# Optimization experiments

Hardware: AMD Instinct MI355X
Metric: run time of the kernel (lower is better)

## Reference

```python
import jax, jax.numpy as jnp
import numpy as np

B, T, d, D = 256, 1024, 4, 32  # batch, seqlen, physical dim, bond dim


def setup_inputs() -> dict:
    key = jax.random.key(0)
    k1, k2, k3, k4 = jax.random.split(key, 4)
    X = jax.random.randint(k1, (B, T), 0, d)  # categorical sequences
    k_core = (d * D * D) ** -0.5
    k_vec = d ** -0.5
    # 'noisy' init: ones + 0.5*gaussian, scaled as in __init__
    core = (k_core * (1.0 + 0.5 * jax.random.normal(k2, (d, D, D)))).astype(jnp.float32)
    left_boundary = (k_vec * (1.0 + 0.5 * jax.random.normal(k3, (D,)))).astype(jnp.float32)
    right_boundary = (k_vec * (1.0 + 0.5 * jax.random.normal(k4, (D,)))).astype(jnp.float32)
    return {"X": X, "core": core, "left_boundary": left_boundary,
            "right_boundary": right_boundary}


def reference(X, core, left_boundary, right_boundary):
    """Batched _log_contract_at: log P(x) per sequence via sequential TT
    contraction with infinity-norm rescaling at every step.
    Returns logprobs of shape [B]."""
    batch = X.shape[0]
    Z0 = jnp.max(jnp.abs(left_boundary))  # vec_norm (inf norm)
    v0 = jnp.broadcast_to(left_boundary / Z0, (batch, D))
    acc0 = jnp.full((batch,), jnp.log(Z0), dtype=left_boundary.dtype)

    def step(carry, x_t):
        v, acc = carry
        M = core[x_t]                              # [B, D, D] gathered cores
        v2 = jnp.einsum('bi,bij->bj', v, M)        # running contraction
        Z = jnp.max(jnp.abs(v2), axis=1)           # per-seq inf norm
        return (v2 / Z[:, None], acc + jnp.log(Z)), None

    (v, acc), _ = jax.lax.scan(step, (v0, acc0), X.T)  # scan over seqlen
    out = jnp.einsum('bi,i->b', v, right_boundary)
    # original: log((exp(acc)*out).abs()**2) == 2*(acc + log|out|)
    logprobs = 2.0 * (acc + jnp.log(jnp.abs(out)))
    return logprobs
```

## Files before the change

### kernel.cpp

```cpp
#include <hip/hip_runtime.h>
#include <math.h>


#define TT_B 256
#define TT_T 1024

typedef __attribute__((ext_vector_type(8))) short bf16x8;
typedef __attribute__((ext_vector_type(4))) float f32x4;

__device__ __forceinline__ unsigned pkbf16(float lo, float hi)
{
    unsigned r;
    asm volatile("v_cvt_pk_bf16_f32 %0, %1, %2" : "=v"(r) : "v"(lo), "v"(hi));
    return r;
}
__device__ __forceinline__ bf16x8 as_bf16x8(int4 v)
{ union { int4 i; bf16x8 h; } u; u.i = v; return u.h; }
__device__ __forceinline__ bf16x8 as_bf16x8u(uint4 v)
{ union { uint4 i; bf16x8 h; } u; u.i = v; return u.h; }

#define MAXD4(D) fmaxf(fmaxf(fabsf(D[0]), fabsf(D[1])), fmaxf(fabsf(D[2]), fabsf(D[3])))

__device__ __forceinline__ int tree_node_lds(const float* __restrict__ Ma,
                                             const float* __restrict__ Mb,
                                             float* __restrict__ Mdst, int lane)
{
    const int p = lane & 15, q = lane >> 4;
    const float4 a00 = *(const float4*)(Mb + p * 36 + 8 * q);
    const float4 a01 = *(const float4*)(Mb + p * 36 + 8 * q + 4);
    const float4 a10 = *(const float4*)(Mb + (16 + p) * 36 + 8 * q);
    const float4 a11 = *(const float4*)(Mb + (16 + p) * 36 + 8 * q + 4);
    int4 aw0, aw1;
    aw0.x = (int)pkbf16(a00.x, a00.y); aw0.y = (int)pkbf16(a00.z, a00.w);
    aw0.z = (int)pkbf16(a01.x, a01.y); aw0.w = (int)pkbf16(a01.z, a01.w);
    aw1.x = (int)pkbf16(a10.x, a10.y); aw1.y = (int)pkbf16(a10.z, a10.w);
    aw1.z = (int)pkbf16(a11.x, a11.y); aw1.w = (int)pkbf16(a11.z, a11.w);
    int4 bw0, bw1;
    bw0.x = (int)pkbf16(Ma[(8*q+0)*36 + p], Ma[(8*q+1)*36 + p]);
    bw0.y = (int)pkbf16(Ma[(8*q+2)*36 + p], Ma[(8*q+3)*36 + p]);
    bw0.z = (int)pkbf16(Ma[(8*q+4)*36 + p], Ma[(8*q+5)*36 + p]);
    bw0.w = (int)pkbf16(Ma[(8*q+6)*36 + p], Ma[(8*q+7)*36 + p]);
    bw1.x = (int)pkbf16(Ma[(8*q+0)*36 + 16 + p], Ma[(8*q+1)*36 + 16 + p]);
    bw1.y = (int)pkbf16(Ma[(8*q+2)*36 + 16 + p], Ma[(8*q+3)*36 + 16 + p]);
    bw1.z = (int)pkbf16(Ma[(8*q+4)*36 + 16 + p], Ma[(8*q+5)*36 + 16 + p]);
    bw1.w = (int)pkbf16(Ma[(8*q+6)*36 + 16 + p], Ma[(8*q+7)*36 + 16 + p]);

    const bf16x8 af0 = as_bf16x8(aw0), af1 = as_bf16x8(aw1);
    const bf16x8 bf0 = as_bf16x8(bw0), bf1 = as_bf16x8(bw1);
    const f32x4 zero = {0.f, 0.f, 0.f, 0.f};
    f32x4 d00 = __builtin_amdgcn_mfma_f32_16x16x32_bf16(af0, bf0, zero, 0, 0, 0);
    f32x4 d01 = __builtin_amdgcn_mfma_f32_16x16x32_bf16(af0, bf1, zero, 0, 0, 0);
    f32x4 d10 = __builtin_amdgcn_mfma_f32_16x16x32_bf16(af1, bf0, zero, 0, 0, 0);
    f32x4 d11 = __builtin_amdgcn_mfma_f32_16x16x32_bf16(af1, bf1, zero, 0, 0, 0);

    float zm = fmaxf(fmaxf(MAXD4(d00), MAXD4(d01)), fmaxf(MAXD4(d10), MAXD4(d11)));
    zm = fmaxf(zm, __shfl_xor(zm,  1));
    zm = fmaxf(zm, __shfl_xor(zm,  2));
    zm = fmaxf(zm, __shfl_xor(zm,  4));
    zm = fmaxf(zm, __shfl_xor(zm,  8));
    zm = fmaxf(zm, __shfl_xor(zm, 16));
    zm = fmaxf(zm, __shfl_xor(zm, 32));
    const int eb = __float_as_int(zm) & 0x7f800000;
    const float s = __int_as_float(0x7F000000 - eb);
#pragma unroll
    for (int t = 0; t < 4; ++t) {
        Mdst[(4*q + t) * 36 + p]           = d00[t] * s;
        Mdst[(4*q + t) * 36 + 16 + p]      = d01[t] * s;
        Mdst[(16 + 4*q + t) * 36 + p]      = d10[t] * s;
        Mdst[(16 + 4*q + t) * 36 + 16 + p] = d11[t] * s;
    }
    return (eb >> 23) - 127;
}

__global__ __launch_bounds__(1024, 1) void tt_fused_kernel(const int* __restrict__ X,
                                                           const float* __restrict__ core,
                                                           const float* __restrict__ Lb,
                                                           const float* __restrict__ Rb,
                                                           float* __restrict__ out)
{
    __shared__ __align__(16) float Ms[24 * 1152];
    __shared__ __align__(16) uint4 Ptab[2048];
    __shared__ int pidx[544];
    __shared__ int kP[16];
    __shared__ int EcA[16];
    __shared__ int kpart[16];

    const int b    = blockIdx.x;
    const int tid  = threadIdx.x;
    const int wid  = tid >> 6;
    const int lane = tid & 63;
    const int p = lane & 15, q = lane >> 4;
    const int g = q, jj = p;

    if (tid < 512) {
        const int2 xv = ((const int2*)(X + (size_t)b * TT_T))[tid];
        pidx[tid] = xv.x * 4 + xv.y;
    } else if (tid < 544) {
        pidx[tid] = 0;
    }
    if (tid < 16) EcA[tid] = 0;
    if (wid >= 8 && wid < 12) {
        const int mi = wid - 8;
        const int r = lane >> 1, hh = (lane & 1) * 16;
        const float4* s4 = (const float4*)(core + mi * 1024 + r * 32 + hh);
        float4 v0 = s4[0], v1 = s4[1], v2 = s4[2], v3 = s4[3];
        float4* d4 = (float4*)(Ms + (16 + mi) * 1152 + r * 36 + hh);
        d4[0] = v0; d4[1] = v1; d4[2] = v2; d4[3] = v3;
    }
    __syncthreads();

    const f32x4 zero = {0.f, 0.f, 0.f, 0.f};

    {
        const float* Pa = Ms + (16 + (wid & 3)) * 1152;
        const float* Pb = Ms + (16 + (wid >> 2)) * 1152;
        const float4 a00 = *(const float4*)(Pb + p * 36 + 8 * q);
        const float4 a01 = *(const float4*)(Pb + p * 36 + 8 * q + 4);
        const float4 a10 = *(const float4*)(Pb + (16 + p) * 36 + 8 * q);
        const float4 a11 = *(const float4*)(Pb + (16 + p) * 36 + 8 * q + 4);
        int4 aw0, aw1;
        aw0.x = (int)pkbf16(a00.x, a00.y); aw0.y = (int)pkbf16(a00.z, a00.w);
        aw0.z = (int)pkbf16(a01.x, a01.y); aw0.w = (int)pkbf16(a01.z, a01.w);
        aw1.x = (int)pkbf16(a10.x, a10.y); aw1.y = (int)pkbf16(a10.z, a10.w);
        aw1.z = (int)pkbf16(a11.x, a11.y); aw1.w = (int)pkbf16(a11.z, a11.w);
        int4 bw0, bw1;
        bw0.x = (int)pkbf16(Pa[(8*q+0)*36 + p], Pa[(8*q+1)*36 + p]);
        bw0.y = (int)pkbf16(Pa[(8*q+2)*36 + p], Pa[(8*q+3)*36 + p]);
        bw0.z = (int)pkbf16(Pa[(8*q+4)*36 + p], Pa[(8*q+5)*36 + p]);
        bw0.w = (int)pkbf16(Pa[(8*q+6)*36 + p], Pa[(8*q+7)*36 + p]);
        bw1.x = (int)pkbf16(Pa[(8*q+0)*36 + 16 + p], Pa[(8*q+1)*36 + 16 + p]);
        bw1.y = (int)pkbf16(Pa[(8*q+2)*36 + 16 + p], Pa[(8*q+3)*36 + 16 + p]);
        bw1.z = (int)pkbf16(Pa[(8*q+4)*36 + 16 + p], Pa[(8*q+5)*36 + 16 + p]);
        bw1.w = (int)pkbf16(Pa[(8*q+6)*36 + 16 + p], Pa[(8*q+7)*36 + 16 + p]);
        const bf16x8 af0 = as_bf16x8(aw0), af1 = as_bf16x8(aw1);
        const bf16x8 bf0 = as_bf16x8(bw0), bf1 = as_bf16x8(bw1);
        f32x4 d00 = __builtin_amdgcn_mfma_f32_16x16x32_bf16(af0, bf0, zero, 0, 0, 0);
        f32x4 d01 = __builtin_amdgcn_mfma_f32_16x16x32_bf16(af0, bf1, zero, 0, 0, 0);
        f32x4 d10 = __builtin_amdgcn_mfma_f32_16x16x32_bf16(af1, bf0, zero, 0, 0, 0);
        f32x4 d11 = __builtin_amdgcn_mfma_f32_16x16x32_bf16(af1, bf1, zero, 0, 0, 0);

        float rs[4], ru[4];
#pragma unroll
        for (int t = 0; t < 4; ++t) {
            rs[t] = fabsf(d00[t]) + fabsf(d01[t]);
            ru[t] = fabsf(d10[t]) + fabsf(d11[t]);
        }
#pragma unroll
        for (int sh = 1; sh <= 8; sh <<= 1) {
#pragma unroll
            for (int t = 0; t < 4; ++t) {
                rs[t] += __shfl_xor(rs[t], sh);
                ru[t] += __shfl_xor(ru[t], sh);
            }
        }
        float mx = fmaxf(fmaxf(fmaxf(rs[0], rs[1]), fmaxf(rs[2], rs[3])),
                         fmaxf(fmaxf(ru[0], ru[1]), fmaxf(ru[2], ru[3])));
        mx = fmaxf(mx, __shfl_xor(mx, 16));
        mx = fmaxf(mx, __shfl_xor(mx, 32));
        const int eb = __float_as_int(mx) & 0x7f800000;
        const float s = __int_as_float(0x7F000000 - eb);
        if (lane == 0) kP[wid] = (eb >> 23) - 127;

        uint4 H0, H1;
        H0.x = pkbf16(d00[0]*s, d00[1]*s);  H0.y = pkbf16(d00[2]*s, d00[3]*s);
        H0.z = pkbf16(d10[0]*s, d10[1]*s);  H0.w = pkbf16(d10[2]*s, d10[3]*s);
        H1.x = pkbf16(d01[0]*s, d01[1]*s);  H1.y = pkbf16(d01[2]*s, d01[3]*s);
        H1.z = pkbf16(d11[0]*s, d11[1]*s);  H1.w = pkbf16(d11[2]*s, d11[3]*s);
        Ptab[wid * 128 + lane]      = H0;
        Ptab[wid * 128 + 64 + lane] = H1;
    }
    __syncthreads();

    int ksum = 0;
    if (tid < 512) ksum = kP[pidx[tid]];
    ksum += __shfl_xor(ksum,  1);
    ksum += __shfl_xor(ksum,  2);
    ksum += __shfl_xor(ksum,  4);
    ksum += __shfl_xor(ksum,  8);
    ksum += __shfl_xor(ksum, 16);
    ksum += __shfl_xor(ksum, 32);
    if (lane == 0) kpart[wid] = ksum;

    const int base = 32 * wid;
    float* Mseg = Ms + wid * 1152;

    unsigned S0w, S1w, S2w, S3w, S4w, S5w, S6w, S7w;
    {
        const unsigned e0 = ((4*g+0 == jj) ? 0x3F80u : 0u) | ((4*g+1 == jj) ? 0x3F800000u : 0u);
        const unsigned e1 = ((4*g+2 == jj) ? 0x3F80u : 0u) | ((4*g+3 == jj) ? 0x3F800000u : 0u);
        S0w = e0; S1w = e1; S2w = 0u; S3w = 0u;
        S4w = 0u; S5w = 0u; S6w = e0; S7w = e1;
    }

    const int m0 = pidx[base];
    uint4 F0c = Ptab[m0 * 128 + lane];
    uint4 F1c = Ptab[m0 * 128 + 64 + lane];

#pragma unroll 1
    for (int t = 0; t < 32; ++t) {
        const int mn = pidx[base + t + 1];
        const uint4 F0n = Ptab[mn * 128 + lane];
        const uint4 F1n = Ptab[mn * 128 + 64 + lane];

        const bf16x8 af0 = as_bf16x8u(F0c);
        const bf16x8 af1 = as_bf16x8u(F1c);
        const bf16x8 sb0 = as_bf16x8u(make_uint4(S0w, S1w, S2w, S3w));
        const bf16x8 sb1 = as_bf16x8u(make_uint4(S4w, S5w, S6w, S7w));
        f32x4 d00 = __builtin_amdgcn_mfma_f32_16x16x32_bf16(af0, sb0, zero, 0, 0, 0);
        f32x4 d01 = __builtin_amdgcn_mfma_f32_16x16x32_bf16(af0, sb1, zero, 0, 0, 0);
        f32x4 d10 = __builtin_amdgcn_mfma_f32_16x16x32_bf16(af1, sb0, zero, 0, 0, 0);
        f32x4 d11 = __builtin_amdgcn_mfma_f32_16x16x32_bf16(af1, sb1, zero, 0, 0, 0);

        if (t == 31) {
#pragma unroll
            for (int u = 0; u < 4; ++u) {
                Mseg[(4*g + u) * 36 + jj]           = d00[u];
                Mseg[(4*g + u) * 36 + 16 + jj]      = d01[u];
                Mseg[(16 + 4*g + u) * 36 + jj]      = d10[u];
                Mseg[(16 + 4*g + u) * 36 + 16 + jj] = d11[u];
            }
        } else {
            S0w = pkbf16(d00[0], d00[1]);  S1w = pkbf16(d00[2], d00[3]);
            S2w = pkbf16(d10[0], d10[1]);  S3w = pkbf16(d10[2], d10[3]);
            S4w = pkbf16(d01[0], d01[1]);  S5w = pkbf16(d01[2], d01[3]);
            S6w = pkbf16(d11[0], d11[1]);  S7w = pkbf16(d11[2], d11[3]);
        }
        F0c = F0n; F1c = F1n;
    }
    __syncthreads();

    if (wid < 8) {
        const int ec = tree_node_lds(Ms + (2*wid) * 1152, Ms + (2*wid + 1) * 1152,
                                     Ms + (16 + wid) * 1152, lane);
        if (lane == 0) EcA[wid] = ec;
    }
    __syncthreads();
    if (wid < 4) {
        const int ec = tree_node_lds(Ms + (16 + 2*wid) * 1152, Ms + (16 + 2*wid + 1) * 1152,
                                     Ms + wid * 1152, lane);
        if (lane == 0) EcA[8 + wid] = ec;
    }
    __syncthreads();
    if (wid < 2) {
        const int ec = tree_node_lds(Ms + (2*wid) * 1152, Ms + (2*wid + 1) * 1152,
                                     Ms + (16 + wid) * 1152, lane);
        if (lane == 0) EcA[12 + wid] = ec;
    }
    __syncthreads();
    int ecL4 = 0;
    if (wid == 0) {
        ecL4 = tree_node_lds(Ms + 16 * 1152, Ms + 17 * 1152, Ms, lane);
    }

    if (wid == 0 && lane < 32) {
        const float* Mt = Ms;
        float v = 0.f;
#pragma unroll 8
        for (int c2 = 0; c2 < 32; ++c2) v = fmaf(Rb[c2], Mt[c2 * 36 + lane], v);
        float pp = v * Lb[lane];
        pp += __shfl_xor(pp,  1);
        pp += __shfl_xor(pp,  2);
        pp += __shfl_xor(pp,  4);
        pp += __shfl_xor(pp,  8);
        pp += __shfl_xor(pp, 16);
        if (lane == 0) {
            int S = ecL4;
#pragma unroll
            for (int w = 0; w < 16; ++w) S += EcA[w] + kpart[w];
            out[b] = 2.0f * ((float)S * 0.6931471805599453f + logf(fabsf(pp)));
        }
    }
}

extern "C" void kernel_launch(void* const* d_in, const int* in_sizes, int n_in,
                              void* d_out, int out_size, void* d_ws, size_t ws_size,
                              hipStream_t stream)
{
    const int*   X    = (const int*)d_in[0];
    const float* core = (const float*)d_in[1];
    const float* Lb   = (const float*)d_in[2];
    const float* Rb   = (const float*)d_in[3];
    float* out = (float*)d_out;

    tt_fused_kernel<<<dim3(256), dim3(1024), 0, stream>>>(X, core, Lb, Rb, out);
}
```

Before: 20.97 us.

## Precompute pair-product table once in a separate kernel and stream it from global memory

The 16-entry table of pairwise core products (as bf16 MFMA fragments, plus exponent shifts) moves out of every block into a one-block pre-kernel that writes it to a global array. The main kernel then fetches fragments with inline-asm global loads, software-pipelined four steps ahead under manual vmcnt waits, so the per-block core load, table MFMAs and one barrier disappear. The cost is an extra kernel launch and a dependency between the two kernels, and the fragment reads now come from L2/global instead of LDS. The hand-written waitcnt depth has to match the number of loads in flight.

```diff
diff --git a/kernel.cpp b/kernel.cpp
--- a/kernel.cpp
+++ b/kernel.cpp
@@ -7,6 +7,9 @@
 
 typedef __attribute__((ext_vector_type(8))) short bf16x8;
 typedef __attribute__((ext_vector_type(4))) float f32x4;
+
+__device__ uint4 g_PT[16 * 2 * 64];
+__device__ int   g_kP[16];
 
 __device__ __forceinline__ unsigned pkbf16(float lo, float hi)
 {
@@ -72,25 +75,134 @@
     return (eb >> 23) - 127;
 }
 
-__global__ __launch_bounds__(1024, 1) void tt_fused_kernel(const int* __restrict__ X,
-                                                           const float* __restrict__ core,
-                                                           const float* __restrict__ Lb,
-                                                           const float* __restrict__ Rb,
-                                                           float* __restrict__ out)
-{
+
+__global__ __launch_bounds__(1024) void tt_pair_kernel(const float* __restrict__ core)
+{
+    __shared__ __align__(16) float Cs[4 * 1152];
+
+    const int tid  = threadIdx.x;
+    const int wid  = tid >> 6;
+    const int lane = tid & 63;
+    const int p = lane & 15, q = lane >> 4;
+
+    if (wid < 4) {
+        const int r = lane >> 1, hh = (lane & 1) * 16;
+        const float4* s4 = (const float4*)(core + wid * 1024 + r * 32 + hh);
+        float4 v0 = s4[0], v1 = s4[1], v2 = s4[2], v3 = s4[3];
+        float4* d4 = (float4*)(Cs + wid * 1152 + r * 36 + hh);
+        d4[0] = v0; d4[1] = v1; d4[2] = v2; d4[3] = v3;
+    }
+    __syncthreads();
+
+    const f32x4 zero = {0.f, 0.f, 0.f, 0.f};
+    const float* Pa = Cs + (wid & 3) * 1152;
+    const float* Pb = Cs + (wid >> 2) * 1152;
+    const float4 a00 = *(const float4*)(Pb + p * 36 + 8 * q);
+    const float4 a01 = *(const float4*)(Pb + p * 36 + 8 * q + 4);
+    const float4 a10 = *(const float4*)(Pb + (16 + p) * 36 + 8 * q);
+    const float4 a11 = *(const float4*)(Pb + (16 + p) * 36 + 8 * q + 4);
+    int4 aw0, aw1;
+    aw0.x = (int)pkbf16(a00.x, a00.y); aw0.y = (int)pkbf16(a00.z, a00.w);
+    aw0.z = (int)pkbf16(a01.x, a01.y); aw0.w = (int)pkbf16(a01.z, a01.w);
+    aw1.x = (int)pkbf16(a10.x, a10.y); aw1.y = (int)pkbf16(a10.z, a10.w);
+    aw1.z = (int)pkbf16(a11.x, a11.y); aw1.w = (int)pkbf16(a11.z, a11.w);
+    int4 bw0, bw1;
+    bw0.x = (int)pkbf16(Pa[(8*q+0)*36 + p], Pa[(8*q+1)*36 + p]);
+    bw0.y = (int)pkbf16(Pa[(8*q+2)*36 + p], Pa[(8*q+3)*36 + p]);
+    bw0.z = (int)pkbf16(Pa[(8*q+4)*36 + p], Pa[(8*q+5)*36 + p]);
+    bw0.w = (int)pkbf16(Pa[(8*q+6)*36 + p], Pa[(8*q+7)*36 + p]);
+    bw1.x = (int)pkbf16(Pa[(8*q+0)*36 + 16 + p], Pa[(8*q+1)*36 + 16 + p]);
+    bw1.y = (int)pkbf16(Pa[(8*q+2)*36 + 16 + p], Pa[(8*q+3)*36 + 16 + p]);
+    bw1.z = (int)pkbf16(Pa[(8*q+4)*36 + 16 + p], Pa[(8*q+5)*36 + 16 + p]);
+    bw1.w = (int)pkbf16(Pa[(8*q+6)*36 + 16 + p], Pa[(8*q+7)*36 + 16 + p]);
+    const bf16x8 af0 = as_bf16x8(aw0), af1 = as_bf16x8(aw1);
+    const bf16x8 bf0 = as_bf16x8(bw0), bf1 = as_bf16x8(bw1);
+    f32x4 d00 = __builtin_amdgcn_mfma_f32_16x16x32_bf16(af0, bf0, zero, 0, 0, 0);
+    f32x4 d01 = __builtin_amdgcn_mfma_f32_16x16x32_bf16(af0, bf1, zero, 0, 0, 0);
+    f32x4 d10 = __builtin_amdgcn_mfma_f32_16x16x32_bf16(af1, bf0, zero, 0, 0, 0);
+    f32x4 d11 = __builtin_amdgcn_mfma_f32_16x16x32_bf16(af1, bf1, zero, 0, 0, 0);
+
+    float rs[4], ru[4];
+#pragma unroll
+    for (int t = 0; t < 4; ++t) {
+        rs[t] = fabsf(d00[t]) + fabsf(d01[t]);
+        ru[t] = fabsf(d10[t]) + fabsf(d11[t]);
+    }
+#pragma unroll
+    for (int sh = 1; sh <= 8; sh <<= 1) {
+#pragma unroll
+        for (int t = 0; t < 4; ++t) {
+            rs[t] += __shfl_xor(rs[t], sh);
+            ru[t] += __shfl_xor(ru[t], sh);
+        }
+    }
+    float mx = fmaxf(fmaxf(fmaxf(rs[0], rs[1]), fmaxf(rs[2], rs[3])),
+                     fmaxf(fmaxf(ru[0], ru[1]), fmaxf(ru[2], ru[3])));
+    mx = fmaxf(mx, __shfl_xor(mx, 16));
+    mx = fmaxf(mx, __shfl_xor(mx, 32));
+    const int eb = __float_as_int(mx) & 0x7f800000;
+    const float s = __int_as_float(0x7F000000 - eb);
+    if (lane == 0) g_kP[wid] = (eb >> 23) - 127;
+
+    uint4 H0, H1;
+    H0.x = pkbf16(d00[0]*s, d00[1]*s);  H0.y = pkbf16(d00[2]*s, d00[3]*s);
+    H0.z = pkbf16(d10[0]*s, d10[1]*s);  H0.w = pkbf16(d10[2]*s, d10[3]*s);
+    H1.x = pkbf16(d01[0]*s, d01[1]*s);  H1.y = pkbf16(d01[2]*s, d01[3]*s);
+    H1.z = pkbf16(d11[0]*s, d11[1]*s);  H1.w = pkbf16(d11[2]*s, d11[3]*s);
+    g_PT[wid * 128 + lane]      = H0;
+    g_PT[wid * 128 + 64 + lane] = H1;
+}
+
+
+#define LOAD2(UB0, UB1, MIDX) do {                                            \
+    const int voff_ = (((MIDX) << 11) | (lane << 4));                         \
+    asm volatile("global_load_dwordx4 %0, %1, %2"             : "=v"(UB0) : "v"(voff_), "s"(qtb)); \
+    asm volatile("global_load_dwordx4 %0, %1, %2 offset:1024" : "=v"(UB1) : "v"(voff_), "s"(qtb)); \
+} while (0)
+
+#define MSTEP(UB0, UB1, MIDX, DO_LAST) do {                                   \
+    const bf16x8 sb0 = as_bf16x8u(make_uint4(S0w, S1w, S2w, S3w));            \
+    const bf16x8 sb1 = as_bf16x8u(make_uint4(S4w, S5w, S6w, S7w));            \
+    asm volatile("s_waitcnt vmcnt(6)" ::: "memory");                          \
+    __builtin_amdgcn_sched_barrier(0);                                        \
+    const bf16x8 af0 = as_bf16x8(UB0);                                        \
+    const bf16x8 af1 = as_bf16x8(UB1);                                        \
+    f32x4 d00 = __builtin_amdgcn_mfma_f32_16x16x32_bf16(af0, sb0, zero, 0, 0, 0); \
+    f32x4 d01 = __builtin_amdgcn_mfma_f32_16x16x32_bf16(af0, sb1, zero, 0, 0, 0); \
+    f32x4 d10 = __builtin_amdgcn_mfma_f32_16x16x32_bf16(af1, sb0, zero, 0, 0, 0); \
+    f32x4 d11 = __builtin_amdgcn_mfma_f32_16x16x32_bf16(af1, sb1, zero, 0, 0, 0); \
+    LOAD2(UB0, UB1, (MIDX));                                                  \
+    if (DO_LAST) {                                                            \
+        _Pragma("unroll") for (int u_ = 0; u_ < 4; ++u_) {                    \
+            Mseg[(4*g + u_) * 36 + jj]           = d00[u_];                   \
+            Mseg[(4*g + u_) * 36 + 16 + jj]      = d01[u_];                   \
+            Mseg[(16 + 4*g + u_) * 36 + jj]      = d10[u_];                   \
+            Mseg[(16 + 4*g + u_) * 36 + 16 + jj] = d11[u_];                   \
+        }                                                                     \
+    } else {                                                                  \
+        S0w = pkbf16(d00[0], d00[1]);  S1w = pkbf16(d00[2], d00[3]);          \
+        S2w = pkbf16(d10[0], d10[1]);  S3w = pkbf16(d10[2], d10[3]);          \
+        S4w = pkbf16(d01[0], d01[1]);  S5w = pkbf16(d01[2], d01[3]);          \
+        S6w = pkbf16(d11[0], d11[1]);  S7w = pkbf16(d11[2], d11[3]);          \
+    }                                                                         \
+} while (0)
+
+__global__ __launch_bounds__(1024, 1) void tt_main_kernel(const int* __restrict__ X,
+                                                          const float* __restrict__ Lb,
+                                                          const float* __restrict__ Rb,
+                                                          float* __restrict__ out)
+{
+    __shared__ __align__(16) int   pidx[544];
     __shared__ __align__(16) float Ms[24 * 1152];
-    __shared__ __align__(16) uint4 Ptab[2048];
-    __shared__ int pidx[544];
-    __shared__ int kP[16];
-    __shared__ int EcA[16];
-    __shared__ int kpart[16];
+    __shared__ int   kPl[16];
+    __shared__ int   EcA[16];
+    __shared__ int   kpart[16];
 
     const int b    = blockIdx.x;
     const int tid  = threadIdx.x;
     const int wid  = tid >> 6;
     const int lane = tid & 63;
-    const int p = lane & 15, q = lane >> 4;
-    const int g = q, jj = p;
+    const int g = lane >> 4, jj = lane & 15;
 
     if (tid < 512) {
         const int2 xv = ((const int2*)(X + (size_t)b * TT_T))[tid];
@@ -98,81 +210,11 @@
     } else if (tid < 544) {
         pidx[tid] = 0;
     }
-    if (tid < 16) EcA[tid] = 0;
-    if (wid >= 8 && wid < 12) {
-        const int mi = wid - 8;
-        const int r = lane >> 1, hh = (lane & 1) * 16;
-        const float4* s4 = (const float4*)(core + mi * 1024 + r * 32 + hh);
-        float4 v0 = s4[0], v1 = s4[1], v2 = s4[2], v3 = s4[3];
-        float4* d4 = (float4*)(Ms + (16 + mi) * 1152 + r * 36 + hh);
-        d4[0] = v0; d4[1] = v1; d4[2] = v2; d4[3] = v3;
-    }
-    __syncthreads();
-
-    const f32x4 zero = {0.f, 0.f, 0.f, 0.f};
-
-    {
-        const float* Pa = Ms + (16 + (wid & 3)) * 1152;
-        const float* Pb = Ms + (16 + (wid >> 2)) * 1152;
-        const float4 a00 = *(const float4*)(Pb + p * 36 + 8 * q);
-        const float4 a01 = *(const float4*)(Pb + p * 36 + 8 * q + 4);
-        const float4 a10 = *(const float4*)(Pb + (16 + p) * 36 + 8 * q);
-        const float4 a11 = *(const float4*)(Pb + (16 + p) * 36 + 8 * q + 4);
-        int4 aw0, aw1;
-        aw0.x = (int)pkbf16(a00.x, a00.y); aw0.y = (int)pkbf16(a00.z, a00.w);
-        aw0.z = (int)pkbf16(a01.x, a01.y); aw0.w = (int)pkbf16(a01.z, a01.w);
-        aw1.x = (int)pkbf16(a10.x, a10.y); aw1.y = (int)pkbf16(a10.z, a10.w);
-        aw1.z = (int)pkbf16(a11.x, a11.y); aw1.w = (int)pkbf16(a11.z, a11.w);
-        int4 bw0, bw1;
-        bw0.x = (int)pkbf16(Pa[(8*q+0)*36 + p], Pa[(8*q+1)*36 + p]);
-        bw0.y = (int)pkbf16(Pa[(8*q+2)*36 + p], Pa[(8*q+3)*36 + p]);
-        bw0.z = (int)pkbf16(Pa[(8*q+4)*36 + p], Pa[(8*q+5)*36 + p]);
-        bw0.w = (int)pkbf16(Pa[(8*q+6)*36 + p], Pa[(8*q+7)*36 + p]);
-        bw1.x = (int)pkbf16(Pa[(8*q+0)*36 + 16 + p], Pa[(8*q+1)*36 + 16 + p]);
-        bw1.y = (int)pkbf16(Pa[(8*q+2)*36 + 16 + p], Pa[(8*q+3)*36 + 16 + p]);
-        bw1.z = (int)pkbf16(Pa[(8*q+4)*36 + 16 + p], Pa[(8*q+5)*36 + 16 + p]);
-        bw1.w = (int)pkbf16(Pa[(8*q+6)*36 + 16 + p], Pa[(8*q+7)*36 + 16 + p]);
-        const bf16x8 af0 = as_bf16x8(aw0), af1 = as_bf16x8(aw1);
-        const bf16x8 bf0 = as_bf16x8(bw0), bf1 = as_bf16x8(bw1);
-        f32x4 d00 = __builtin_amdgcn_mfma_f32_16x16x32_bf16(af0, bf0, zero, 0, 0, 0);
-        f32x4 d01 = __builtin_amdgcn_mfma_f32_16x16x32_bf16(af0, bf1, zero, 0, 0, 0);
-        f32x4 d10 = __builtin_amdgcn_mfma_f32_16x16x32_bf16(af1, bf0, zero, 0, 0, 0);
-        f32x4 d11 = __builtin_amdgcn_mfma_f32_16x16x32_bf16(af1, bf1, zero, 0, 0, 0);
-
-        float rs[4], ru[4];
-#pragma unroll
-        for (int t = 0; t < 4; ++t) {
-            rs[t] = fabsf(d00[t]) + fabsf(d01[t]);
-            ru[t] = fabsf(d10[t]) + fabsf(d11[t]);
-        }
-#pragma unroll
-        for (int sh = 1; sh <= 8; sh <<= 1) {
-#pragma unroll
-            for (int t = 0; t < 4; ++t) {
-                rs[t] += __shfl_xor(rs[t], sh);
-                ru[t] += __shfl_xor(ru[t], sh);
-            }
-        }
-        float mx = fmaxf(fmaxf(fmaxf(rs[0], rs[1]), fmaxf(rs[2], rs[3])),
-                         fmaxf(fmaxf(ru[0], ru[1]), fmaxf(ru[2], ru[3])));
-        mx = fmaxf(mx, __shfl_xor(mx, 16));
-        mx = fmaxf(mx, __shfl_xor(mx, 32));
-        const int eb = __float_as_int(mx) & 0x7f800000;
-        const float s = __int_as_float(0x7F000000 - eb);
-        if (lane == 0) kP[wid] = (eb >> 23) - 127;
-
-        uint4 H0, H1;
-        H0.x = pkbf16(d00[0]*s, d00[1]*s);  H0.y = pkbf16(d00[2]*s, d00[3]*s);
-        H0.z = pkbf16(d10[0]*s, d10[1]*s);  H0.w = pkbf16(d10[2]*s, d10[3]*s);
-        H1.x = pkbf16(d01[0]*s, d01[1]*s);  H1.y = pkbf16(d01[2]*s, d01[3]*s);
-        H1.z = pkbf16(d11[0]*s, d11[1]*s);  H1.w = pkbf16(d11[2]*s, d11[3]*s);
-        Ptab[wid * 128 + lane]      = H0;
-        Ptab[wid * 128 + 64 + lane] = H1;
-    }
+    if (tid < 16) { kPl[tid] = g_kP[tid]; EcA[tid] = 0; }
     __syncthreads();
 
     int ksum = 0;
-    if (tid < 512) ksum = kP[pidx[tid]];
+    if (tid < 512) ksum = kPl[pidx[tid]];
     ksum += __shfl_xor(ksum,  1);
     ksum += __shfl_xor(ksum,  2);
     ksum += __shfl_xor(ksum,  4);
@@ -181,7 +223,11 @@
     ksum += __shfl_xor(ksum, 32);
     if (lane == 0) kpart[wid] = ksum;
 
-    const int base = 32 * wid;
+    const uint4* qtb = g_PT;
+    const f32x4 zero = {0.f, 0.f, 0.f, 0.f};
+
+    const int base4 = 8 * wid;
+    const int4* idxs4 = (const int4*)pidx;
     float* Mseg = Ms + wid * 1152;
 
     unsigned S0w, S1w, S2w, S3w, S4w, S5w, S6w, S7w;
@@ -192,41 +238,28 @@
         S4w = 0u; S5w = 0u; S6w = e0; S7w = e1;
     }
 
-    const int m0 = pidx[base];
-    uint4 F0c = Ptab[m0 * 128 + lane];
-    uint4 F1c = Ptab[m0 * 128 + 64 + lane];
+    int4 Ba0, Ba1, Bb0, Bb1, Bc0, Bc1, Bd0, Bd1;
+    {
+        const int4 m0 = idxs4[base4];
+        LOAD2(Ba0, Ba1, m0.x);
+        LOAD2(Bb0, Bb1, m0.y);
+        LOAD2(Bc0, Bc1, m0.z);
+        LOAD2(Bd0, Bd1, m0.w);
+    }
+    int4 mqc = idxs4[base4 + 1];
 
 #pragma unroll 1
-    for (int t = 0; t < 32; ++t) {
-        const int mn = pidx[base + t + 1];
-        const uint4 F0n = Ptab[mn * 128 + lane];
-        const uint4 F1n = Ptab[mn * 128 + 64 + lane];
-
-        const bf16x8 af0 = as_bf16x8u(F0c);
-        const bf16x8 af1 = as_bf16x8u(F1c);
-        const bf16x8 sb0 = as_bf16x8u(make_uint4(S0w, S1w, S2w, S3w));
-        const bf16x8 sb1 = as_bf16x8u(make_uint4(S4w, S5w, S6w, S7w));
-        f32x4 d00 = __builtin_amdgcn_mfma_f32_16x16x32_bf16(af0, sb0, zero, 0, 0, 0);
-        f32x4 d01 = __builtin_amdgcn_mfma_f32_16x16x32_bf16(af0, sb1, zero, 0, 0, 0);
-        f32x4 d10 = __builtin_amdgcn_mfma_f32_16x16x32_bf16(af1, sb0, zero, 0, 0, 0);
-        f32x4 d11 = __builtin_amdgcn_mfma_f32_16x16x32_bf16(af1, sb1, zero, 0, 0, 0);
-
-        if (t == 31) {
-#pragma unroll
-            for (int u = 0; u < 4; ++u) {
-                Mseg[(4*g + u) * 36 + jj]           = d00[u];
-                Mseg[(4*g + u) * 36 + 16 + jj]      = d01[u];
-                Mseg[(16 + 4*g + u) * 36 + jj]      = d10[u];
-                Mseg[(16 + 4*g + u) * 36 + 16 + jj] = d11[u];
-            }
-        } else {
-            S0w = pkbf16(d00[0], d00[1]);  S1w = pkbf16(d00[2], d00[3]);
-            S2w = pkbf16(d10[0], d10[1]);  S3w = pkbf16(d10[2], d10[3]);
-            S4w = pkbf16(d01[0], d01[1]);  S5w = pkbf16(d01[2], d01[3]);
-            S6w = pkbf16(d11[0], d11[1]);  S7w = pkbf16(d11[2], d11[3]);
-        }
-        F0c = F0n; F1c = F1n;
-    }
+    for (int J = 0; J < 8; ++J) {
+        const int4 mq_nx = idxs4[base4 + J + 2];
+        const bool lt = (J == 7);
+        MSTEP(Ba0, Ba1, mqc.x, 0);
+        MSTEP(Bb0, Bb1, mqc.y, 0);
+        MSTEP(Bc0, Bc1, mqc.z, 0);
+        MSTEP(Bd0, Bd1, mqc.w, lt);
+        mqc = mq_nx;
+    }
+
+    asm volatile("s_waitcnt vmcnt(0)" ::: "memory");
     __syncthreads();
 
     if (wid < 8) {
@@ -282,5 +315,6 @@
     const float* Rb   = (const float*)d_in[3];
     float* out = (float*)d_out;
 
-    tt_fused_kernel<<<dim3(256), dim3(1024), 0, stream>>>(X, core, Lb, Rb, out);
-}
+    tt_pair_kernel<<<dim3(1),   dim3(1024), 0, stream>>>(core);
+    tt_main_kernel<<<dim3(256), dim3(1024), 0, stream>>>(X, Lb, Rb, out);
+}
```

Measured after the change: 23.89 us. 1.14x slower.

## Halve block to 512 threads with 64-step segments and shallower reduction tree

Applied to the files above, without the earlier changes.

Each block now uses 8 waves instead of 16. Each wave walks a 64-step segment of the chain instead of 32, and the pairwise-product table is built by each wave handling two entries. Shared memory shrinks: the tree reduction reuses Ptab as scratch and has one fewer level, with launch bounds allowing several blocks per CU. This cuts LDS footprint, barrier count and tree depth so more blocks can run at once. In exchange, the serial MFMA chain per wave becomes twice as long.

```diff
diff --git a/kernel.cpp b/kernel.cpp
--- a/kernel.cpp
+++ b/kernel.cpp
@@ -72,18 +72,18 @@
     return (eb >> 23) - 127;
 }
 
-__global__ __launch_bounds__(1024, 1) void tt_fused_kernel(const int* __restrict__ X,
-                                                           const float* __restrict__ core,
-                                                           const float* __restrict__ Lb,
-                                                           const float* __restrict__ Rb,
-                                                           float* __restrict__ out)
-{
-    __shared__ __align__(16) float Ms[24 * 1152];
+__global__ __launch_bounds__(512, 4) void tt_fused_kernel(const int* __restrict__ X,
+                                                          const float* __restrict__ core,
+                                                          const float* __restrict__ Lb,
+                                                          const float* __restrict__ Rb,
+                                                          float* __restrict__ out)
+{
+    __shared__ __align__(16) float Ms[8 * 1152];
     __shared__ __align__(16) uint4 Ptab[2048];
-    __shared__ int pidx[544];
+    __shared__ int pidx[528];
     __shared__ int kP[16];
-    __shared__ int EcA[16];
-    __shared__ int kpart[16];
+    __shared__ int EcA[8];
+    __shared__ int kpart[8];
 
     const int b    = blockIdx.x;
     const int tid  = threadIdx.x;
@@ -92,28 +92,29 @@
     const int p = lane & 15, q = lane >> 4;
     const int g = q, jj = p;
 
-    if (tid < 512) {
+    {
         const int2 xv = ((const int2*)(X + (size_t)b * TT_T))[tid];
         pidx[tid] = xv.x * 4 + xv.y;
-    } else if (tid < 544) {
-        pidx[tid] = 0;
-    }
-    if (tid < 16) EcA[tid] = 0;
-    if (wid >= 8 && wid < 12) {
-        const int mi = wid - 8;
+    }
+    if (tid < 16) { pidx[512 + tid] = 0; }
+    if (tid < 8)  { EcA[tid] = 0; }
+    if (wid >= 4) {
+        const int mi = wid - 4;
         const int r = lane >> 1, hh = (lane & 1) * 16;
         const float4* s4 = (const float4*)(core + mi * 1024 + r * 32 + hh);
         float4 v0 = s4[0], v1 = s4[1], v2 = s4[2], v3 = s4[3];
-        float4* d4 = (float4*)(Ms + (16 + mi) * 1152 + r * 36 + hh);
+        float4* d4 = (float4*)(Ms + (4 + mi) * 1152 + r * 36 + hh);
         d4[0] = v0; d4[1] = v1; d4[2] = v2; d4[3] = v3;
     }
     __syncthreads();
 
     const f32x4 zero = {0.f, 0.f, 0.f, 0.f};
 
-    {
-        const float* Pa = Ms + (16 + (wid & 3)) * 1152;
-        const float* Pb = Ms + (16 + (wid >> 2)) * 1152;
+#pragma unroll
+    for (int pp2 = 0; pp2 < 2; ++pp2) {
+        const int m = 2 * wid + pp2;
+        const float* Pa = Ms + (4 + (m & 3)) * 1152;
+        const float* Pb = Ms + (4 + (m >> 2)) * 1152;
         const float4 a00 = *(const float4*)(Pb + p * 36 + 8 * q);
         const float4 a01 = *(const float4*)(Pb + p * 36 + 8 * q + 4);
         const float4 a10 = *(const float4*)(Pb + (16 + p) * 36 + 8 * q);
@@ -159,20 +160,19 @@
         mx = fmaxf(mx, __shfl_xor(mx, 32));
         const int eb = __float_as_int(mx) & 0x7f800000;
         const float s = __int_as_float(0x7F000000 - eb);
-        if (lane == 0) kP[wid] = (eb >> 23) - 127;
+        if (lane == 0) kP[m] = (eb >> 23) - 127;
 
         uint4 H0, H1;
         H0.x = pkbf16(d00[0]*s, d00[1]*s);  H0.y = pkbf16(d00[2]*s, d00[3]*s);
         H0.z = pkbf16(d10[0]*s, d10[1]*s);  H0.w = pkbf16(d10[2]*s, d10[3]*s);
         H1.x = pkbf16(d01[0]*s, d01[1]*s);  H1.y = pkbf16(d01[2]*s, d01[3]*s);
         H1.z = pkbf16(d11[0]*s, d11[1]*s);  H1.w = pkbf16(d11[2]*s, d11[3]*s);
-        Ptab[wid * 128 + lane]      = H0;
-        Ptab[wid * 128 + 64 + lane] = H1;
-    }
-    __syncthreads();
-
-    int ksum = 0;
-    if (tid < 512) ksum = kP[pidx[tid]];
+        Ptab[m * 128 + lane]      = H0;
+        Ptab[m * 128 + 64 + lane] = H1;
+    }
+    __syncthreads();
+
+    int ksum = kP[pidx[tid]];
     ksum += __shfl_xor(ksum,  1);
     ksum += __shfl_xor(ksum,  2);
     ksum += __shfl_xor(ksum,  4);
@@ -181,7 +181,7 @@
     ksum += __shfl_xor(ksum, 32);
     if (lane == 0) kpart[wid] = ksum;
 
-    const int base = 32 * wid;
+    const int base = 64 * wid;
     float* Mseg = Ms + wid * 1152;
 
     unsigned S0w, S1w, S2w, S3w, S4w, S5w, S6w, S7w;
@@ -197,7 +197,7 @@
     uint4 F1c = Ptab[m0 * 128 + 64 + lane];
 
 #pragma unroll 1
-    for (int t = 0; t < 32; ++t) {
+    for (int t = 0; t < 64; ++t) {
         const int mn = pidx[base + t + 1];
         const uint4 F0n = Ptab[mn * 128 + lane];
         const uint4 F1n = Ptab[mn * 128 + 64 + lane];
@@ -211,7 +211,7 @@
         f32x4 d10 = __builtin_amdgcn_mfma_f32_16x16x32_bf16(af1, sb0, zero, 0, 0, 0);
         f32x4 d11 = __builtin_amdgcn_mfma_f32_16x16x32_bf16(af1, sb1, zero, 0, 0, 0);
 
-        if (t == 31) {
+        if (t == 63) {
 #pragma unroll
             for (int u = 0; u < 4; ++u) {
                 Mseg[(4*g + u) * 36 + jj]           = d00[u];
@@ -229,34 +229,29 @@
     }
     __syncthreads();
 
-    if (wid < 8) {
+    float* Mt = (float*)Ptab;
+    if (wid < 4) {
         const int ec = tree_node_lds(Ms + (2*wid) * 1152, Ms + (2*wid + 1) * 1152,
-                                     Ms + (16 + wid) * 1152, lane);
+                                     Mt + wid * 1152, lane);
         if (lane == 0) EcA[wid] = ec;
     }
     __syncthreads();
-    if (wid < 4) {
-        const int ec = tree_node_lds(Ms + (16 + 2*wid) * 1152, Ms + (16 + 2*wid + 1) * 1152,
-                                     Ms + wid * 1152, lane);
-        if (lane == 0) EcA[8 + wid] = ec;
-    }
-    __syncthreads();
     if (wid < 2) {
-        const int ec = tree_node_lds(Ms + (2*wid) * 1152, Ms + (2*wid + 1) * 1152,
-                                     Ms + (16 + wid) * 1152, lane);
-        if (lane == 0) EcA[12 + wid] = ec;
-    }
-    __syncthreads();
-    int ecL4 = 0;
+        const int ec = tree_node_lds(Mt + (2*wid) * 1152, Mt + (2*wid + 1) * 1152,
+                                     Mt + (4 + wid) * 1152, lane);
+        if (lane == 0) EcA[4 + wid] = ec;
+    }
+    __syncthreads();
+    int ecL3 = 0;
     if (wid == 0) {
-        ecL4 = tree_node_lds(Ms + 16 * 1152, Ms + 17 * 1152, Ms, lane);
+        ecL3 = tree_node_lds(Mt + 4 * 1152, Mt + 5 * 1152, Mt + 6 * 1152, lane);
     }
 
     if (wid == 0 && lane < 32) {
-        const float* Mt = Ms;
+        const float* Mf = Mt + 6 * 1152;
         float v = 0.f;
 #pragma unroll 8
-        for (int c2 = 0; c2 < 32; ++c2) v = fmaf(Rb[c2], Mt[c2 * 36 + lane], v);
+        for (int c2 = 0; c2 < 32; ++c2) v = fmaf(Rb[c2], Mf[c2 * 36 + lane], v);
         float pp = v * Lb[lane];
         pp += __shfl_xor(pp,  1);
         pp += __shfl_xor(pp,  2);
@@ -264,9 +259,11 @@
         pp += __shfl_xor(pp,  8);
         pp += __shfl_xor(pp, 16);
         if (lane == 0) {
-            int S = ecL4;
-#pragma unroll
-            for (int w = 0; w < 16; ++w) S += EcA[w] + kpart[w];
+            int S = ecL3;
+#pragma unroll
+            for (int w = 0; w < 6; ++w) S += EcA[w];
+#pragma unroll
+            for (int w = 0; w < 8; ++w) S += kpart[w];
             out[b] = 2.0f * ((float)S * 0.6931471805599453f + logf(fabsf(pp)));
         }
     }
@@ -282,5 +279,5 @@
     const float* Rb   = (const float*)d_in[3];
     float* out = (float*)d_out;
 
-    tt_fused_kernel<<<dim3(256), dim3(1024), 0, stream>>>(X, core, Lb, Rb, out);
-}
+    tt_fused_kernel<<<dim3(256), dim3(512), 0, stream>>>(X, core, Lb, Rb, out);
+}
```

New measurement: 21.50 us. 1.02x slower.
